# Kernel tuning notes

Hardware: AMD Instinct MI355X
Metric: run time of the kernel (lower is better)

Reference implementation:

```python
import jax, jax.numpy as jnp
import numpy as np
import math

NUM_BUCKETS = 32
MAX_DISTANCE = 128
N_HEADS = 16
D_KV = 64
D_MODEL = 1024


def _relative_position_bucket(relative_position, num_buckets=NUM_BUCKETS, max_distance=MAX_DISTANCE):
    # bidirectional (encoder) variant
    num_buckets = num_buckets // 2
    relative_buckets = (relative_position > 0).astype(jnp.int32) * num_buckets
    relative_position = jnp.abs(relative_position)
    max_exact = num_buckets // 2
    is_small = relative_position < max_exact
    # avoid log(0); masked by is_small anyway
    rp = jnp.maximum(relative_position, 1).astype(jnp.float32)
    rel_if_large = max_exact + (
        jnp.log(rp / max_exact) / math.log(max_distance / max_exact) * (num_buckets - max_exact)
    ).astype(jnp.int32)
    rel_if_large = jnp.minimum(rel_if_large, num_buckets - 1)
    relative_buckets = relative_buckets + jnp.where(is_small, relative_position, rel_if_large)
    return relative_buckets


def compute_bias(rel_bias, q_len, k_len):
    context = jnp.arange(q_len, dtype=jnp.int32)[:, None]
    memory = jnp.arange(k_len, dtype=jnp.int32)[None, :]
    buckets = _relative_position_bucket(memory - context)  # [q,k]
    values = rel_bias[buckets]                              # [q,k,H]
    return jnp.transpose(values, (2, 0, 1))[None]           # [1,H,q,k]


def setup_inputs() -> dict:
    key = jax.random.key(0)
    k1, k2, k3, k4 = jax.random.split(key, 4)
    B, S = 2, 2048
    hidden_states = jax.random.normal(k1, (B, S, D_MODEL), dtype=jnp.float32)
    attention_mask = jnp.ones((B, S), dtype=jnp.int32)
    w_qkv = jax.random.normal(k2, (3 * D_MODEL, D_MODEL), dtype=jnp.float32) * 0.02
    rel_bias = jax.random.normal(k3, (NUM_BUCKETS, N_HEADS), dtype=jnp.float32)
    w_o = jax.random.normal(k4, (D_MODEL, D_MODEL), dtype=jnp.float32) * 0.02
    return {"hidden_states": hidden_states, "attention_mask": attention_mask,
            "w_qkv": w_qkv, "rel_bias": rel_bias, "w_o": w_o}


def reference(hidden_states, attention_mask, w_qkv, rel_bias, w_o):
    B, S, _ = hidden_states.shape
    n, c = N_HEADS, D_KV
    qkv = hidden_states @ w_qkv.T                      # [B,S,3*inner]
    q, k, v = jnp.split(qkv, 3, axis=-1)
    q = q.reshape(B, S, n, c)
    k = k.reshape(B, S, n, c)
    v = v.reshape(B, S, n, c)
    attn_bias = jnp.broadcast_to(compute_bias(rel_bias, S, S), (B, n, S, S))
    mask = attention_mask.reshape(B, 1, 1, S)
    mask_val = jnp.finfo(q.dtype).min
    attn_bias = jnp.where(mask == 0, mask_val, attn_bias)
    attn = jnp.einsum('binc,bjnc->bnij', q, k) + attn_bias   # no 1/sqrt(d) scale in T5
    attn = jax.nn.softmax(attn.astype(jnp.float32), axis=-1).astype(q.dtype)
    x = jnp.einsum('bnij,bjnc->binc', attn, v)
    x = x.reshape(B, S, n * c)
    return x @ w_o.T
```

## Files before the change

### kernel.cpp

```cpp
#include <hip/hip_runtime.h>
#include <stdint.h>

typedef __attribute__((ext_vector_type(4))) float f32x4;
typedef __attribute__((ext_vector_type(8))) short short8;
typedef __attribute__((ext_vector_type(4))) short short4v;
typedef __attribute__((ext_vector_type(2))) unsigned uint2v;

__device__ __forceinline__ short f2bf(float f) {
    union { float f; unsigned u; } x; x.f = f;
    return (short)((x.u + 0x7fffu + ((x.u >> 16) & 1u)) >> 16);
}

__device__ __forceinline__ unsigned cvt_pk_bf16(float lo, float hi) {
    unsigned r;
    asm("v_cvt_pk_bf16_f32 %0, %1, %2" : "=v"(r) : "v"(lo), "v"(hi));
    return r;
}

__device__ __forceinline__ float fexp2(float x) {
#if __has_builtin(__builtin_amdgcn_exp2f)
    return __builtin_amdgcn_exp2f(x);
#else
    return exp2f(x);
#endif
}

#define MFMA16(a, b, c) __builtin_amdgcn_mfma_f32_16x16x32_bf16((a), (b), (c), 0, 0, 0)

__device__ __forceinline__ void gload16(const void* g, void* l) {
    __builtin_amdgcn_global_load_lds((const __attribute__((address_space(1))) void*)g,
                                     (__attribute__((address_space(3))) void*)l, 16, 0, 0);
}

__global__ __launch_bounds__(256) void cast_all(const float* __restrict__ h,
                                                const float* __restrict__ wq,
                                                const float* __restrict__ wo,
                                                short* __restrict__ hb,
                                                short* __restrict__ wqb,
                                                short* __restrict__ wob) {
    int i = blockIdx.x * 256 + threadIdx.x;
    const float* s;
    short* d;
    int j;
    if (i < 524288) { s = h; d = hb; j = i; }
    else if (i < 917504) { s = wq; d = wqb; j = i - 524288; }
    else { s = wo; d = wob; j = i - 917504; }
    float4 a = ((const float4*)s)[j * 2];
    float4 b = ((const float4*)s)[j * 2 + 1];
    short8 o;
    o[0] = f2bf(a.x); o[1] = f2bf(a.y); o[2] = f2bf(a.z); o[3] = f2bf(a.w);
    o[4] = f2bf(b.x); o[5] = f2bf(b.y); o[6] = f2bf(b.z); o[7] = f2bf(b.w);
    ((short8*)d)[j] = o;
}

template <int OUT_BF16, int QSCALE, int VFUSE>
__global__ __launch_bounds__(512, 2) void gemm8p(const short* __restrict__ A,
                                                 const short* __restrict__ B,
                                                 void* __restrict__ Cout,
                                                 short* __restrict__ vt,
                                                 int M, int N, int K) {
    __shared__ short lds[2][4][8192];
    const int t = threadIdx.x;
    const int l = t & 63, w = t >> 6;
    const int lr = l & 15, lg = l >> 4;
    const int wr = w >> 2, wc = w & 3;
    const int wg = blockIdx.y * 12 + blockIdx.x;
    const int xcd = wg & 7, ii = wg >> 3;
    const int byp = (xcd >> 1) * 4 + ii / 6;
    const int bxp = (xcd & 1) * 6 + ii % 6;
    const int m0 = byp * 256, n0 = bxp * 256;
    const int nt = K >> 6, nh = nt << 2;

    const int sr0 = t >> 2;
    const int scc = ((t & 3) ^ ((sr0 >> 1) & 3)) * 8;
    const short* As0 = A + (size_t)(m0 + sr0) * K + scc;
    const short* As1 = A + (size_t)(m0 + sr0 + 128) * K + scc;
    const short* Bs0 = B + (size_t)(n0 + sr0) * K + scc;
    const short* Bs1 = B + (size_t)(n0 + sr0 + 128) * K + scc;
    short* ldsb = &lds[0][0][0];

    auto stageH = [&](int H) {
        int Tp = H >> 2, pos = H & 3;
        int kb = Tp * 64 + ((pos <= 1) ? 32 : 0);
        short* dst = ldsb + ((Tp & 1) * 4 + pos) * 8192 + t * 8;
        if (pos & 1) {
            gload16(As0 + kb, dst);
            gload16(As1 + kb, dst + 4096);
        } else {
            gload16(Bs0 + kb, dst);
            gload16(Bs1 + kb, dst + 4096);
        }
    };

    int aoff[8], boff[4];
    #pragma unroll
    for (int mi = 0; mi < 8; ++mi) {
        int row = wr * 128 + mi * 16 + lr;
        aoff[mi] = row * 32 + (lg ^ ((row >> 1) & 3)) * 8;
    }
    #pragma unroll
    for (int ni = 0; ni < 4; ++ni) {
        int row = wc * 64 + ni * 16 + lr;
        boff[ni] = row * 32 + (lg ^ ((row >> 1) & 3)) * 8;
    }

    f32x4 acc[8][4] = {};

    for (int H = 0; H < 7; ++H) stageH(H);
    asm volatile("s_waitcnt vmcnt(6)" ::: "memory");
    __builtin_amdgcn_s_barrier();

    for (int T = 0; T < nt; ++T) {
        const short* rbase = ldsb + (T & 1) * 32768;
        const short* B1b = rbase;
        const short* A1b = rbase + 8192;
        const short* B0b = rbase + 16384;
        const short* A0b = rbase + 24576;
        const int Hs = (T << 2) + 7;
        short8 a[4], b[4];

        #pragma unroll
        for (int i = 0; i < 4; ++i) a[i] = *(const short8*)(A1b + aoff[i]);
        #pragma unroll
        for (int i = 0; i < 4; ++i) b[i] = *(const short8*)(B1b + boff[i]);
        if (Hs < nh) stageH(Hs);
        __builtin_amdgcn_sched_barrier(0);
        __builtin_amdgcn_s_barrier();
        asm volatile("s_waitcnt lgkmcnt(0)" ::: "memory");
        __builtin_amdgcn_sched_barrier(0);
        __builtin_amdgcn_s_setprio(1);
        #pragma unroll
        for (int mi = 0; mi < 4; ++mi)
            #pragma unroll
            for (int ni = 0; ni < 4; ++ni)
                acc[mi][ni] = MFMA16(a[mi], b[ni], acc[mi][ni]);
        __builtin_amdgcn_s_setprio(0);
        __builtin_amdgcn_sched_barrier(0);
        __builtin_amdgcn_s_barrier();

        #pragma unroll
        for (int i = 0; i < 4; ++i) a[i] = *(const short8*)(A1b + aoff[4 + i]);
        if (Hs + 1 < nh) stageH(Hs + 1);
        __builtin_amdgcn_sched_barrier(0);
        __builtin_amdgcn_s_barrier();
        asm volatile("s_waitcnt lgkmcnt(0)" ::: "memory");
        __builtin_amdgcn_sched_barrier(0);
        __builtin_amdgcn_s_setprio(1);
        #pragma unroll
        for (int mi = 0; mi < 4; ++mi)
            #pragma unroll
            for (int ni = 0; ni < 4; ++ni)
                acc[4 + mi][ni] = MFMA16(a[mi], b[ni], acc[4 + mi][ni]);
        __builtin_amdgcn_s_setprio(0);
        __builtin_amdgcn_sched_barrier(0);
        __builtin_amdgcn_s_barrier();

        #pragma unroll
        for (int i = 0; i < 4; ++i) a[i] = *(const short8*)(A0b + aoff[i]);
        #pragma unroll
        for (int i = 0; i < 4; ++i) b[i] = *(const short8*)(B0b + boff[i]);
        if (Hs + 2 < nh) stageH(Hs + 2);
        __builtin_amdgcn_sched_barrier(0);
        __builtin_amdgcn_s_barrier();
        asm volatile("s_waitcnt lgkmcnt(0)" ::: "memory");
        __builtin_amdgcn_sched_barrier(0);
        __builtin_amdgcn_s_setprio(1);
        #pragma unroll
        for (int mi = 0; mi < 4; ++mi)
            #pragma unroll
            for (int ni = 0; ni < 4; ++ni)
                acc[mi][ni] = MFMA16(a[mi], b[ni], acc[mi][ni]);
        __builtin_amdgcn_s_setprio(0);
        __builtin_amdgcn_sched_barrier(0);
        __builtin_amdgcn_s_barrier();

        #pragma unroll
        for (int i = 0; i < 4; ++i) a[i] = *(const short8*)(A0b + aoff[4 + i]);
        if (Hs + 3 < nh) stageH(Hs + 3);
        __builtin_amdgcn_sched_barrier(0);
        __builtin_amdgcn_s_barrier();
        asm volatile("s_waitcnt lgkmcnt(0)" ::: "memory");
        __builtin_amdgcn_sched_barrier(0);
        __builtin_amdgcn_s_setprio(1);
        #pragma unroll
        for (int mi = 0; mi < 4; ++mi)
            #pragma unroll
            for (int ni = 0; ni < 4; ++ni)
                acc[4 + mi][ni] = MFMA16(a[mi], b[ni], acc[4 + mi][ni]);
        __builtin_amdgcn_s_setprio(0);
        if (T < nt - 2) {
            asm volatile("s_waitcnt vmcnt(6)" ::: "memory");
        } else if (T == nt - 2) {
            asm volatile("s_waitcnt vmcnt(0)" ::: "memory");
        }
        __builtin_amdgcn_sched_barrier(0);
        __builtin_amdgcn_s_barrier();
    }

    if (VFUSE && n0 >= 2048) {
        #pragma unroll
        for (int mi = 0; mi < 8; ++mi)
            #pragma unroll
            for (int ni = 0; ni < 4; ++ni) {
                int nn = n0 + wc * 64 + ni * 16 + lr;
                int h = (nn - 2048) >> 6, dd = (nn - 2048) & 63;
                int mm = m0 + wr * 128 + mi * 16 + lg * 4;
                int bb = mm >> 11, s = mm & 2047;
                short4v ov;
                #pragma unroll
                for (int rr = 0; rr < 4; ++rr) ov[rr] = f2bf(acc[mi][ni][rr]);
                *(short4v*)(vt + ((size_t)(bb * 16 + h) * 64 + dd) * 2048 + s) = ov;
            }
        return;
    }
    const float qs = (QSCALE && n0 < 1024) ? 1.4426950408889634f : 1.0f;
    #pragma unroll
    for (int mi = 0; mi < 8; ++mi)
        #pragma unroll
        for (int ni = 0; ni < 4; ++ni)
            #pragma unroll
            for (int rr = 0; rr < 4; ++rr) {
                int mm = m0 + wr * 128 + mi * 16 + lg * 4 + rr;
                int nn = n0 + wc * 64 + ni * 16 + lr;
                float v = acc[mi][ni][rr] * qs;
                if (OUT_BF16) ((short*)Cout)[(size_t)mm * N + nn] = f2bf(v);
                else ((float*)Cout)[(size_t)mm * N + nn] = v;
            }
}

template <int OUT_BF16>
__global__ __launch_bounds__(256) void gemm_bt(const short* __restrict__ A,
                                               const short* __restrict__ B,
                                               void* __restrict__ Cout,
                                               int M, int N, int K) {
    __shared__ short sA[4096];
    __shared__ short sB[4096];
    const int t = threadIdx.x;
    const int l = t & 63, w = t >> 6;
    const int lr = l & 15, lg = l >> 4;
    const int wg = blockIdx.y * 8 + blockIdx.x;
    const int xcd = wg & 7, ii = wg >> 3;
    const int m0 = (xcd * 4 + (ii >> 3)) * 128, n0 = (ii & 7) * 128;
    const int wm = (w >> 1) * 64, wn = (w & 1) * 64;
    const int c0 = w * 64 + l, c1 = c0 + 256;
    const short* Ap0 = A + (size_t)(m0 + (c0 >> 2)) * K + (c0 & 3) * 8;
    const short* Ap1 = A + (size_t)(m0 + (c1 >> 2)) * K + (c1 & 3) * 8;
    const short* Bp0 = B + (size_t)(n0 + (c0 >> 2)) * K + (c0 & 3) * 8;
    const short* Bp1 = B + (size_t)(n0 + (c1 >> 2)) * K + (c1 & 3) * 8;
    short* lA0 = sA + w * 512;
    short* lA1 = sA + 2048 + w * 512;
    short* lB0 = sB + w * 512;
    short* lB1 = sB + 2048 + w * 512;
    f32x4 acc[4][4] = {};
    for (int k0 = 0; k0 < K; k0 += 32) {
        gload16(Ap0 + k0, lA0);
        gload16(Ap1 + k0, lA1);
        gload16(Bp0 + k0, lB0);
        gload16(Bp1 + k0, lB1);
        __syncthreads();
        short8 af[4], bfr[4];
        #pragma unroll
        for (int m = 0; m < 4; ++m) af[m] = *(const short8*)&sA[(wm + m * 16 + lr) * 32 + lg * 8];
        #pragma unroll
        for (int n = 0; n < 4; ++n) bfr[n] = *(const short8*)&sB[(wn + n * 16 + lr) * 32 + lg * 8];
        #pragma unroll
        for (int m = 0; m < 4; ++m)
            #pragma unroll
            for (int n = 0; n < 4; ++n)
                acc[m][n] = MFMA16(af[m], bfr[n], acc[m][n]);
        __syncthreads();
    }
    #pragma unroll
    for (int m = 0; m < 4; ++m)
        #pragma unroll
        for (int n = 0; n < 4; ++n)
            #pragma unroll
            for (int r = 0; r < 4; ++r) {
                int mm = m0 + wm + m * 16 + lg * 4 + r;
                int nn = n0 + wn + n * 16 + lr;
                float v = acc[m][n][r];
                if (OUT_BF16) ((short*)Cout)[(size_t)mm * N + nn] = f2bf(v);
                else ((float*)Cout)[(size_t)mm * N + nn] = v;
            }
}

__global__ __launch_bounds__(512, 4) void attn_kernel(const short* __restrict__ qkv,
                                                      const short* __restrict__ vt,
                                                      const int* __restrict__ amask,
                                                      const float* __restrict__ rel_bias,
                                                      short* __restrict__ xout) {
    __shared__ float tbl[340];
    __shared__ short sK[4096];
    __shared__ short sV[4096];
    __shared__ short sP[8][16][72];
    __shared__ int mflags[32];
    const int t = threadIdx.x;
    const int l = t & 63, w = t >> 6;
    const int lr = l & 15, lg = l >> 4;
    const int wg = blockIdx.y * 16 + blockIdx.x;
    const int swz = (wg & 7) * 64 + (wg >> 3);
    const int qt = swz & 15, bh = swz >> 4;
    const int b = bh >> 4, h = bh & 15;
    const int q0 = qt * 128 + w * 16;
    const float LOG2E = 1.4426950408889634f;

    if (t < 32) mflags[t] = ~0;
    if (t < 337) {
        int idx = t;
        int d = idx - 168;
        int a = d < 0 ? -d : d;
        int fb = a < 8 ? a
                 : (a < 12 ? 8 : a < 16 ? 9 : a < 23 ? 10 : a < 32 ? 11
                    : a < 46 ? 12 : a < 64 ? 13 : a < 91 ? 14 : 15);
        int bk = (d > 0 ? 16 : 0) + fb;
        tbl[idx] = rel_bias[bk * 16 + h] * LOG2E;
    }
    const float rbp = rel_bias[31 * 16 + h] * LOG2E;
    const float rbn = rel_bias[15 * 16 + h] * LOG2E;

    short8 qf[2];
    #pragma unroll
    for (int ds = 0; ds < 2; ++ds)
        qf[ds] = *(const short8*)(qkv + (size_t)(b * 2048 + q0 + lr) * 3072 + h * 64 + ds * 32 + lg * 8);

    const int4 ma = ((const int4*)(amask + b * 2048))[t];

    const int srow = t >> 3;
    const int scp = ((t & 7) ^ (srow & 7)) * 8;
    const short* kgp = qkv + (size_t)(b * 2048 + srow) * 3072 + 1024 + h * 64 + scp;
    const short* vgp = vt + ((size_t)bh * 64 + srow) * 2048 + scp;
    short* dK = sK + t * 8;
    short* dV = sV + t * 8;
    const int sw8 = (lr & 7) * 8;
    const int ibb = -q0 + lg * 4 - lr + 168;

    __syncthreads();
    int mok = ma.x & ma.y & ma.z & ma.w;
    if (mok == 0) atomicAnd(&mflags[t >> 4], 0);

    f32x4 o[4] = {};
    float mreg = -1e30f, lreg = 0.f;

    for (int kt = 0; kt < 2048; kt += 64) {
        gload16(kgp + (size_t)kt * 3072, dK);
        gload16(vgp + kt, dV);
        __syncthreads();

        f32x4 pe[4];
        #pragma unroll
        for (int ct = 0; ct < 4; ++ct) {
            f32x4 z = {};
            #pragma unroll
            for (int ds = 0; ds < 2; ++ds) {
                short8 kf = *(const short8*)&sK[(ct * 16 + lr) * 64 + ((ds * 32 + lg * 8) ^ sw8)];
                z = MFMA16(kf, qf[ds], z);
            }
            pe[ct] = z;
        }

        float cb;
        if (kt >= q0 + 106) {
            cb = rbp;
        } else if (kt + 63 <= q0 - 91) {
            cb = rbn;
        } else {
            cb = 0.f;
            const int ib = kt + ibb;
            #pragma unroll
            for (int ct = 0; ct < 4; ++ct)
                #pragma unroll
                for (int r = 0; r < 4; ++r)
                    pe[ct][r] += tbl[ib + ct * 16 + r];
        }

        float t0 = fmaxf(fmaxf(pe[0][0], pe[0][1]), fmaxf(pe[0][2], pe[0][3]));
        float t1 = fmaxf(fmaxf(pe[1][0], pe[1][1]), fmaxf(pe[1][2], pe[1][3]));
        float t2 = fmaxf(fmaxf(pe[2][0], pe[2][1]), fmaxf(pe[2][2], pe[2][3]));
        float t3 = fmaxf(fmaxf(pe[3][0], pe[3][1]), fmaxf(pe[3][2], pe[3][3]));
        float lmax = fmaxf(fmaxf(t0, t1), fmaxf(t2, t3));
        if (__any(lmax > mreg - cb + 11.5f)) {
            float rm = fmaxf(lmax, __shfl_xor(lmax, 16));
            rm = fmaxf(rm, __shfl_xor(rm, 32));
            float mnew = fmaxf(mreg, rm + cb);
            float alpha = fexp2(mreg - mnew);
            lreg *= alpha;
            #pragma unroll
            for (int dt = 0; dt < 4; ++dt)
                #pragma unroll
                for (int r = 0; r < 4; ++r)
                    o[dt][r] *= alpha;
            mreg = mnew;
        }
        const float madj = mreg - cb;
        const int tok = mflags[kt >> 6];
        float rs = 0.f;
        if (tok) {
            #pragma unroll
            for (int ct = 0; ct < 4; ++ct) {
                float p[4];
                #pragma unroll
                for (int r = 0; r < 4; ++r) {
                    float pv = fexp2(pe[ct][r] - madj);
                    p[r] = pv;
                    rs += pv;
                }
                uint2v pk;
                pk[0] = cvt_pk_bf16(p[0], p[1]);
                pk[1] = cvt_pk_bf16(p[2], p[3]);
                *(uint2v*)&sP[w][lr][ct * 16 + lg * 4] = pk;
            }
        } else {
            const int4* mp = (const int4*)(amask + b * 2048 + kt);
            #pragma unroll
            for (int ct = 0; ct < 4; ++ct) {
                int4 cm = mp[ct * 4 + lg];
                float p[4];
                #pragma unroll
                for (int r = 0; r < 4; ++r) {
                    float pv = fexp2(pe[ct][r] - madj);
                    pv = ((const int*)&cm)[r] ? pv : 0.f;
                    p[r] = pv;
                    rs += pv;
                }
                uint2v pk;
                pk[0] = cvt_pk_bf16(p[0], p[1]);
                pk[1] = cvt_pk_bf16(p[2], p[3]);
                *(uint2v*)&sP[w][lr][ct * 16 + lg * 4] = pk;
            }
        }
        lreg += rs;

        #pragma unroll
        for (int kk = 0; kk < 2; ++kk) {
            short8 pf = *(const short8*)&sP[w][lr][kk * 32 + lg * 8];
            #pragma unroll
            for (int dt = 0; dt < 4; ++dt) {
                short8 vf = *(const short8*)&sV[(dt * 16 + lr) * 64 + ((kk * 32 + lg * 8) ^ sw8)];
                o[dt] = MFMA16(vf, pf, o[dt]);
            }
        }
        __syncthreads();
    }

    float lsum = lreg + __shfl_xor(lreg, 16);
    lsum += __shfl_xor(lsum, 32);
    const float inv = 1.0f / lsum;
    #pragma unroll
    for (int dt = 0; dt < 4; ++dt) {
        short4v ov;
        #pragma unroll
        for (int r = 0; r < 4; ++r) ov[r] = f2bf(o[dt][r] * inv);
        *(short4v*)(xout + (size_t)(b * 2048 + q0 + lr) * 1024 + h * 64 + dt * 16 + lg * 4) = ov;
    }
}

extern "C" void kernel_launch(void* const* d_in, const int* in_sizes, int n_in,
                              void* d_out, int out_size, void* d_ws, size_t ws_size,
                              hipStream_t stream) {
    const float* hidden = (const float*)d_in[0];
    const int* amask = (const int*)d_in[1];
    const float* w_qkv = (const float*)d_in[2];
    const float* rel_bias = (const float*)d_in[3];
    const float* w_o = (const float*)d_in[4];
    if (ws_size < 58720256) return;
    char* ws = (char*)d_ws;
    short* hidden_bf = (short*)(ws + 0);
    short* wqkv_bf   = (short*)(ws + 8388608);
    short* wo_bf     = (short*)(ws + 14680064);
    short* qkv       = (short*)(ws + 16777216);
    short* vt        = (short*)(ws + 41943040);
    short* xbuf      = (short*)(ws + 50331648);

    cast_all<<<4096, 256, 0, stream>>>(hidden, w_qkv, w_o, hidden_bf, wqkv_bf, wo_bf);
    gemm8p<1, 1, 1><<<dim3(12, 16), 512, 0, stream>>>(hidden_bf, wqkv_bf, qkv, vt, 4096, 3072, 1024);
    attn_kernel<<<dim3(16, 32), 512, 0, stream>>>(qkv, vt, amask, rel_bias, xbuf);
    gemm_bt<0><<<dim3(8, 32), 256, 0, stream>>>(xbuf, wo_bf, d_out, 4096, 1024, 1024);
}
```

Measured before the change: 128.9 us.

## Retile QKV GEMM to 256x192 blocks with simpler double-buffered K pipeline

```diff
diff --git a/kernel.cpp b/kernel.cpp
--- a/kernel.cpp
+++ b/kernel.cpp
@@ -53,77 +53,76 @@
     ((short8*)d)[j] = o;
 }
 
-template <int OUT_BF16, int QSCALE, int VFUSE>
-__global__ __launch_bounds__(512, 2) void gemm8p(const short* __restrict__ A,
-                                                 const short* __restrict__ B,
-                                                 void* __restrict__ Cout,
-                                                 short* __restrict__ vt,
-                                                 int M, int N, int K) {
-    __shared__ short lds[2][4][8192];
+__global__ __launch_bounds__(512, 2) void gemm192(const short* __restrict__ A,
+                                                  const short* __restrict__ B,
+                                                  short* __restrict__ Cout,
+                                                  short* __restrict__ vt,
+                                                  int M, int N, int K) {
+    __shared__ short lds[2][28672];
     const int t = threadIdx.x;
     const int l = t & 63, w = t >> 6;
     const int lr = l & 15, lg = l >> 4;
     const int wr = w >> 2, wc = w & 3;
-    const int wg = blockIdx.y * 12 + blockIdx.x;
+    const int wg = blockIdx.y * 16 + blockIdx.x;
     const int xcd = wg & 7, ii = wg >> 3;
-    const int byp = (xcd >> 1) * 4 + ii / 6;
-    const int bxp = (xcd & 1) * 6 + ii % 6;
-    const int m0 = byp * 256, n0 = bxp * 256;
-    const int nt = K >> 6, nh = nt << 2;
-
-    const int sr0 = t >> 2;
-    const int scc = ((t & 3) ^ ((sr0 >> 1) & 3)) * 8;
-    const short* As0 = A + (size_t)(m0 + sr0) * K + scc;
-    const short* As1 = A + (size_t)(m0 + sr0 + 128) * K + scc;
-    const short* Bs0 = B + (size_t)(n0 + sr0) * K + scc;
-    const short* Bs1 = B + (size_t)(n0 + sr0 + 128) * K + scc;
-    short* ldsb = &lds[0][0][0];
-
-    auto stageH = [&](int H) {
-        int Tp = H >> 2, pos = H & 3;
-        int kb = Tp * 64 + ((pos <= 1) ? 32 : 0);
-        short* dst = ldsb + ((Tp & 1) * 4 + pos) * 8192 + t * 8;
-        if (pos & 1) {
-            gload16(As0 + kb, dst);
-            gload16(As1 + kb, dst + 4096);
-        } else {
-            gload16(Bs0 + kb, dst);
-            gload16(Bs1 + kb, dst + 4096);
-        }
-    };
-
-    int aoff[8], boff[4];
+    const int m0 = ((xcd >> 1) * 4 + (ii >> 3)) * 256;
+    const int n0 = ((xcd & 1) * 8 + (ii & 7)) * 192;
+    const int nt = K >> 6;
+
+    const int srow = t >> 3;
+    const int sc = ((t & 7) ^ (srow & 7)) * 8;
+    const short* Ab = A + (size_t)(m0 + srow) * K + sc;
+    const short* Bb = B + (size_t)(n0 + srow) * K + sc;
+    const size_t rK64 = (size_t)64 * K;
+
+    int aoff[2][8], boff[2][3];
     #pragma unroll
     for (int mi = 0; mi < 8; ++mi) {
         int row = wr * 128 + mi * 16 + lr;
-        aoff[mi] = row * 32 + (lg ^ ((row >> 1) & 3)) * 8;
-    }
-    #pragma unroll
-    for (int ni = 0; ni < 4; ++ni) {
-        int row = wc * 64 + ni * 16 + lr;
-        boff[ni] = row * 32 + (lg ^ ((row >> 1) & 3)) * 8;
-    }
-
-    f32x4 acc[8][4] = {};
-
-    for (int H = 0; H < 7; ++H) stageH(H);
-    asm volatile("s_waitcnt vmcnt(6)" ::: "memory");
+        aoff[0][mi] = row * 64 + ((lg ^ (row & 7)) * 8);
+        aoff[1][mi] = row * 64 + (((4 + lg) ^ (row & 7)) * 8);
+    }
+    #pragma unroll
+    for (int ni = 0; ni < 3; ++ni) {
+        int row = wc * 48 + ni * 16 + lr;
+        boff[0][ni] = row * 64 + ((lg ^ (row & 7)) * 8);
+        boff[1][ni] = row * 64 + (((4 + lg) ^ (row & 7)) * 8);
+    }
+
+    f32x4 acc[8][3] = {};
+
+    {
+        short* dA = &lds[0][0] + t * 8;
+        short* dB = &lds[0][16384] + t * 8;
+        gload16(Bb, dB);
+        gload16(Bb + rK64, dB + 4096);
+        gload16(Bb + 2 * rK64, dB + 8192);
+        gload16(Ab, dA);
+        gload16(Ab + rK64, dA + 4096);
+        gload16(Ab + 2 * rK64, dA + 8192);
+        gload16(Ab + 3 * rK64, dA + 12288);
+    }
+    asm volatile("s_waitcnt vmcnt(0)" ::: "memory");
     __builtin_amdgcn_s_barrier();
 
     for (int T = 0; T < nt; ++T) {
-        const short* rbase = ldsb + (T & 1) * 32768;
-        const short* B1b = rbase;
-        const short* A1b = rbase + 8192;
-        const short* B0b = rbase + 16384;
-        const short* A0b = rbase + 24576;
-        const int Hs = (T << 2) + 7;
-        short8 a[4], b[4];
-
-        #pragma unroll
-        for (int i = 0; i < 4; ++i) a[i] = *(const short8*)(A1b + aoff[i]);
-        #pragma unroll
-        for (int i = 0; i < 4; ++i) b[i] = *(const short8*)(B1b + boff[i]);
-        if (Hs < nh) stageH(Hs);
+        const short* Abuf = &lds[T & 1][0];
+        const short* Bbuf = &lds[T & 1][16384];
+        short* nA = &lds[(T & 1) ^ 1][0] + t * 8;
+        short* nB = &lds[(T & 1) ^ 1][16384] + t * 8;
+        const bool more = (T + 1 < nt);
+        const int kb = (T + 1) * 64;
+        short8 a[4], b[3];
+
+        #pragma unroll
+        for (int i = 0; i < 4; ++i) a[i] = *(const short8*)(Abuf + aoff[1][i]);
+        #pragma unroll
+        for (int i = 0; i < 3; ++i) b[i] = *(const short8*)(Bbuf + boff[1][i]);
+        if (more) {
+            gload16(Bb + kb, nB);
+            gload16(Bb + rK64 + kb, nB + 4096);
+            gload16(Bb + 2 * rK64 + kb, nB + 8192);
+        }
         __builtin_amdgcn_sched_barrier(0);
         __builtin_amdgcn_s_barrier();
         asm volatile("s_waitcnt lgkmcnt(0)" ::: "memory");
@@ -132,15 +131,18 @@
         #pragma unroll
         for (int mi = 0; mi < 4; ++mi)
             #pragma unroll
-            for (int ni = 0; ni < 4; ++ni)
+            for (int ni = 0; ni < 3; ++ni)
                 acc[mi][ni] = MFMA16(a[mi], b[ni], acc[mi][ni]);
         __builtin_amdgcn_s_setprio(0);
         __builtin_amdgcn_sched_barrier(0);
         __builtin_amdgcn_s_barrier();
 
         #pragma unroll
-        for (int i = 0; i < 4; ++i) a[i] = *(const short8*)(A1b + aoff[4 + i]);
-        if (Hs + 1 < nh) stageH(Hs + 1);
+        for (int i = 0; i < 4; ++i) a[i] = *(const short8*)(Abuf + aoff[1][4 + i]);
+        if (more) {
+            gload16(Ab + kb, nA);
+            gload16(Ab + rK64 + kb, nA + 4096);
+        }
         __builtin_amdgcn_sched_barrier(0);
         __builtin_amdgcn_s_barrier();
         asm volatile("s_waitcnt lgkmcnt(0)" ::: "memory");
@@ -149,17 +151,20 @@
         #pragma unroll
         for (int mi = 0; mi < 4; ++mi)
             #pragma unroll
-            for (int ni = 0; ni < 4; ++ni)
+            for (int ni = 0; ni < 3; ++ni)
                 acc[4 + mi][ni] = MFMA16(a[mi], b[ni], acc[4 + mi][ni]);
         __builtin_amdgcn_s_setprio(0);
         __builtin_amdgcn_sched_barrier(0);
         __builtin_amdgcn_s_barrier();
 
         #pragma unroll
-        for (int i = 0; i < 4; ++i) a[i] = *(const short8*)(A0b + aoff[i]);
-        #pragma unroll
-        for (int i = 0; i < 4; ++i) b[i] = *(const short8*)(B0b + boff[i]);
-        if (Hs + 2 < nh) stageH(Hs + 2);
+        for (int i = 0; i < 4; ++i) a[i] = *(const short8*)(Abuf + aoff[0][i]);
+        #pragma unroll
+        for (int i = 0; i < 3; ++i) b[i] = *(const short8*)(Bbuf + boff[0][i]);
+        if (more) {
+            gload16(Ab + 2 * rK64 + kb, nA + 8192);
+            gload16(Ab + 3 * rK64 + kb, nA + 12288);
+        }
         __builtin_amdgcn_sched_barrier(0);
         __builtin_amdgcn_s_barrier();
         asm volatile("s_waitcnt lgkmcnt(0)" ::: "memory");
@@ -168,15 +173,14 @@
         #pragma unroll
         for (int mi = 0; mi < 4; ++mi)
             #pragma unroll
-            for (int ni = 0; ni < 4; ++ni)
+            for (int ni = 0; ni < 3; ++ni)
                 acc[mi][ni] = MFMA16(a[mi], b[ni], acc[mi][ni]);
         __builtin_amdgcn_s_setprio(0);
         __builtin_amdgcn_sched_barrier(0);
         __builtin_amdgcn_s_barrier();
 
         #pragma unroll
-        for (int i = 0; i < 4; ++i) a[i] = *(const short8*)(A0b + aoff[4 + i]);
-        if (Hs + 3 < nh) stageH(Hs + 3);
+        for (int i = 0; i < 4; ++i) a[i] = *(const short8*)(Abuf + aoff[0][4 + i]);
         __builtin_amdgcn_sched_barrier(0);
         __builtin_amdgcn_s_barrier();
         asm volatile("s_waitcnt lgkmcnt(0)" ::: "memory");
@@ -185,47 +189,36 @@
         #pragma unroll
         for (int mi = 0; mi < 4; ++mi)
             #pragma unroll
-            for (int ni = 0; ni < 4; ++ni)
+            for (int ni = 0; ni < 3; ++ni)
                 acc[4 + mi][ni] = MFMA16(a[mi], b[ni], acc[4 + mi][ni]);
         __builtin_amdgcn_s_setprio(0);
-        if (T < nt - 2) {
-            asm volatile("s_waitcnt vmcnt(6)" ::: "memory");
-        } else if (T == nt - 2) {
-            asm volatile("s_waitcnt vmcnt(0)" ::: "memory");
-        }
-        __builtin_amdgcn_sched_barrier(0);
-        __builtin_amdgcn_s_barrier();
-    }
-
-    if (VFUSE && n0 >= 2048) {
-        #pragma unroll
-        for (int mi = 0; mi < 8; ++mi)
-            #pragma unroll
-            for (int ni = 0; ni < 4; ++ni) {
-                int nn = n0 + wc * 64 + ni * 16 + lr;
-                int h = (nn - 2048) >> 6, dd = (nn - 2048) & 63;
-                int mm = m0 + wr * 128 + mi * 16 + lg * 4;
-                int bb = mm >> 11, s = mm & 2047;
+        if (more) asm volatile("s_waitcnt vmcnt(0)" ::: "memory");
+        __builtin_amdgcn_sched_barrier(0);
+        __builtin_amdgcn_s_barrier();
+    }
+
+    const float LOG2E = 1.4426950408889634f;
+    #pragma unroll
+    for (int mi = 0; mi < 8; ++mi)
+        #pragma unroll
+        for (int ni = 0; ni < 3; ++ni) {
+            const int col0 = n0 + wc * 48 + ni * 16;
+            const int mmb = m0 + wr * 128 + mi * 16 + lg * 4;
+            if (col0 >= 2048) {
+                const int h = (col0 - 2048) >> 6;
+                const int dd = ((col0 - 2048) & 63) + lr;
+                const int bb = mmb >> 11, s = mmb & 2047;
                 short4v ov;
                 #pragma unroll
                 for (int rr = 0; rr < 4; ++rr) ov[rr] = f2bf(acc[mi][ni][rr]);
                 *(short4v*)(vt + ((size_t)(bb * 16 + h) * 64 + dd) * 2048 + s) = ov;
-            }
-        return;
-    }
-    const float qs = (QSCALE && n0 < 1024) ? 1.4426950408889634f : 1.0f;
-    #pragma unroll
-    for (int mi = 0; mi < 8; ++mi)
-        #pragma unroll
-        for (int ni = 0; ni < 4; ++ni)
-            #pragma unroll
-            for (int rr = 0; rr < 4; ++rr) {
-                int mm = m0 + wr * 128 + mi * 16 + lg * 4 + rr;
-                int nn = n0 + wc * 64 + ni * 16 + lr;
-                float v = acc[mi][ni][rr] * qs;
-                if (OUT_BF16) ((short*)Cout)[(size_t)mm * N + nn] = f2bf(v);
-                else ((float*)Cout)[(size_t)mm * N + nn] = v;
-            }
+            } else {
+                const float qs = (col0 < 1024) ? LOG2E : 1.0f;
+                #pragma unroll
+                for (int rr = 0; rr < 4; ++rr)
+                    Cout[(size_t)(mmb + rr) * N + col0 + lr] = f2bf(acc[mi][ni][rr] * qs);
+            }
+        }
 }
 
 template <int OUT_BF16>
@@ -472,7 +465,7 @@
     short* xbuf      = (short*)(ws + 50331648);
 
     cast_all<<<4096, 256, 0, stream>>>(hidden, w_qkv, w_o, hidden_bf, wqkv_bf, wo_bf);
-    gemm8p<1, 1, 1><<<dim3(12, 16), 512, 0, stream>>>(hidden_bf, wqkv_bf, qkv, vt, 4096, 3072, 1024);
+    gemm192<<<dim3(16, 16), 512, 0, stream>>>(hidden_bf, wqkv_bf, qkv, vt, 4096, 3072, 1024);
     attn_kernel<<<dim3(16, 32), 512, 0, stream>>>(qkv, vt, amask, rel_bias, xbuf);
     gemm_bt<0><<<dim3(8, 32), 256, 0, stream>>>(xbuf, wo_bf, d_out, 4096, 1024, 1024);
 }
```

Measured after the change: 123.9 us. 1.04x faster.
